# Optimization experiments

Measured on AMD Instinct MI355X. Metric: run time of the kernel, lower is better.

## Reference

```python
import jax, jax.numpy as jnp
import numpy as np

HIDDEN = 1024
HEADS = 16
HEAD_DIM = HIDDEN // HEADS  # 64
MLP_HIDDEN = int(HIDDEN * 4.0)  # 4096
B, L = 2, 2048
EPS_LN = 1e-6
EPS_RMS = 1e-6


def setup_inputs() -> dict:
    key = jax.random.key(0)
    ks = jax.random.split(key, 12)
    s = 0.02
    return {
        "x": jax.random.normal(ks[0], (B, L, HIDDEN), jnp.float32),
        "vec": jax.random.normal(ks[1], (B, HIDDEN), jnp.float32),
        "pe": jax.random.normal(ks[2], (1, 1, L, HEAD_DIM // 2, 2, 2), jnp.float32),
        "w_mod": jax.random.normal(ks[3], (HIDDEN, 3 * HIDDEN), jnp.float32) * s,
        "b_mod": jnp.zeros((3 * HIDDEN,), jnp.float32),
        "w1": jax.random.normal(ks[4], (HIDDEN, 3 * HIDDEN + MLP_HIDDEN), jnp.float32) * s,
        "b1": jnp.zeros((3 * HIDDEN + MLP_HIDDEN,), jnp.float32),
        "w_mlp": jax.random.normal(ks[5], (MLP_HIDDEN, HIDDEN), jnp.float32) * s,
        "b_mlp": jnp.zeros((HIDDEN,), jnp.float32),
        "w2": jax.random.normal(ks[6], (2 * HIDDEN, HIDDEN), jnp.float32) * s,
        "b2": jnp.zeros((HIDDEN,), jnp.float32),
        "q_scale": jnp.ones((HEAD_DIM,), jnp.float32),
        "k_scale": jnp.ones((HEAD_DIM,), jnp.float32),
    }


def _layernorm(x, eps=EPS_LN):
    m = jnp.mean(x, axis=-1, keepdims=True)
    v = jnp.mean(jnp.square(x - m), axis=-1, keepdims=True)
    return (x - m) * jax.lax.rsqrt(v + eps)


def _rmsnorm(x, scale, eps=EPS_RMS):
    rrms = jax.lax.rsqrt(jnp.mean(jnp.square(x), axis=-1, keepdims=True) + eps)
    return x * rrms * scale


def _apply_rope(t, pe):
    # t: [B,H,L,D]; pe: [1,1,L,D//2,2,2]
    t_ = t.reshape(*t.shape[:-1], -1, 1, 2)  # [B,H,L,D//2,1,2]
    out = pe[..., 0] * t_[..., 0] + pe[..., 1] * t_[..., 1]  # [B,H,L,D//2,2]
    return out.reshape(t.shape)


def reference(x, vec, pe, w_mod, b_mod, w1, b1, w_mlp, b_mlp, w2, b2, q_scale, k_scale):
    # adaLN modulation: silu(vec) -> Dense(3*dim) -> shift, scale, gate
    mod = (jax.nn.silu(vec) @ w_mod + b_mod)[:, None, :]  # [B,1,3H]
    shift, scale, gate = jnp.split(mod, 3, axis=-1)
    x_mod = (1.0 + scale) * _layernorm(x) + shift
    # fused QKV + MLP projection
    h = x_mod @ w1 + b1  # [B,L,3H+MH]
    qkv, mlp = h[..., : 3 * HIDDEN], h[..., 3 * HIDDEN :]
    qkv = qkv.reshape(x.shape[0], x.shape[1], 3, HEADS, HEAD_DIM)
    qkv = jnp.transpose(qkv, (2, 0, 3, 1, 4))  # [3,B,H,L,D]
    q, k, v = qkv[0], qkv[1], qkv[2]
    # QK-RMSNorm per head-dim
    q = _rmsnorm(q, q_scale)
    k = _rmsnorm(k, k_scale)
    # RoPE
    q = _apply_rope(q, pe)
    k = _apply_rope(k, pe)
    # attention
    scores = jnp.einsum("bhqd,bhkd->bhqk", q, k) * (HEAD_DIM ** -0.5)
    probs = jax.nn.softmax(scores, axis=-1)
    attn = jnp.einsum("bhqk,bhkd->bhqd", probs, v)
    attn = jnp.transpose(attn, (0, 2, 1, 3)).reshape(x.shape[0], x.shape[1], HIDDEN)
    # mlp branch (Dense with tanh activation per source) + fused output proj
    mlp_out = jnp.tanh(mlp @ w_mlp + b_mlp)
    out = jnp.concatenate([attn, mlp_out], axis=-1) @ w2 + b2
    return x + gate * out
```

## Files before the change

### kernel.cpp

```cpp
#include <hip/hip_runtime.h>
#include <stdint.h>


#define HID  1024
#define NH   16
#define HD   64
#define MLP  4096
#define D1   7168
#define DQKV 3072
#define DCAT 2048
#define BB   2
#define LL   2048
#define TOK  4096

typedef __attribute__((ext_vector_type(8))) short    bf16x8;
typedef __attribute__((ext_vector_type(4))) float    f32x4;
typedef __attribute__((ext_vector_type(4))) unsigned int u32x4;

__device__ __forceinline__ float b2f(unsigned short u) {
    unsigned int v = ((unsigned int)u) << 16;
    float f; __builtin_memcpy(&f, &v, 4); return f;
}
__device__ __forceinline__ unsigned short f2b(float f) {
    unsigned int v; __builtin_memcpy(&v, &f, 4);
    unsigned int r = (v + 0x7FFFu + ((v >> 16) & 1u)) >> 16;
    return (unsigned short)r;
}
__device__ __forceinline__ unsigned int pkbf2(float a, float b) {
    unsigned int ua, ub;
    __builtin_memcpy(&ua, &a, 4); __builtin_memcpy(&ub, &b, 4);
    return ((ua + 0x8000u) >> 16) | ((ub + 0x8000u) & 0xFFFF0000u);
}
__device__ __forceinline__ void gl_lds16(const unsigned short* g, unsigned short* l) {
    __builtin_amdgcn_global_load_lds(
        (const __attribute__((address_space(1))) unsigned int*)(g),
        (__attribute__((address_space(3))) unsigned int*)(l), 16, 0, 0);
}

__global__ void k_transpose_cvt(const float* __restrict__ in,
                                unsigned short* __restrict__ out, int R, int C) {
    __shared__ float tile[32][33];
    int bx = blockIdx.x, by = blockIdx.y;
    int tx = threadIdx.x, ty = threadIdx.y;
    #pragma unroll
    for (int i = 0; i < 4; i++) {
        int r = by * 32 + ty + i * 8;
        int c = bx * 32 + tx;
        tile[ty + i * 8][tx] = in[(size_t)r * C + c];
    }
    __syncthreads();
    #pragma unroll
    for (int i = 0; i < 4; i++) {
        int ro = bx * 32 + ty + i * 8;
        int co = by * 32 + tx;
        out[(size_t)ro * R + co] = f2b(tile[tx][ty + i * 8]);
    }
}

__global__ void k_mod(const float* __restrict__ vec,
                      const float* __restrict__ w_mod,
                      const float* __restrict__ b_mod,
                      float* __restrict__ mod) {
    __shared__ float sv[HID];
    __shared__ float red[8][32];
    int b = blockIdx.y, t = threadIdx.x;
    for (int j = t; j < HID; j += 256) {
        float v = vec[b * HID + j];
        sv[j] = v / (1.0f + __expf(-v));
    }
    __syncthreads();
    int n0 = blockIdx.x * 32;
    int on = t & 31, ks = t >> 5;
    float acc = 0.f;
    const float* wp = w_mod + (size_t)(ks * 128) * 3072 + n0 + on;
    #pragma unroll 4
    for (int k = 0; k < 128; k++) acc += sv[ks * 128 + k] * wp[(size_t)k * 3072];
    red[ks][on] = acc;
    __syncthreads();
    if (t < 32) {
        float s = 0.f;
        #pragma unroll
        for (int i = 0; i < 8; i++) s += red[i][t];
        mod[b * 3072 + n0 + t] = s + b_mod[n0 + t];
    }
}

__global__ void k_lnmod(const float* __restrict__ x,
                        const float* __restrict__ mod,
                        unsigned short* __restrict__ xmod) {
    int tok = blockIdx.x;
    int t = threadIdx.x;
    int b = tok >> 11;
    float4 v4 = *(const float4*)(x + (size_t)tok * HID + t * 4);
    float v0 = v4.x, v1 = v4.y, v2 = v4.z, v3 = v4.w;
    float s  = v0 + v1 + v2 + v3;
    float sq = v0*v0 + v1*v1 + v2*v2 + v3*v3;
    for (int off = 1; off < 64; off <<= 1) {
        s  += __shfl_xor(s,  off);
        sq += __shfl_xor(sq, off);
    }
    __shared__ float ls[4], lq[4];
    int w = t >> 6;
    if ((t & 63) == 0) { ls[w] = s; lq[w] = sq; }
    __syncthreads();
    s  = ls[0] + ls[1] + ls[2] + ls[3];
    sq = lq[0] + lq[1] + lq[2] + lq[3];
    float mean = s * (1.0f / HID);
    float var  = sq * (1.0f / HID) - mean * mean;
    float rstd = rsqrtf(var + 1e-6f);
    const float* mb = mod + b * 3072;
    float y[4] = {v0, v1, v2, v3};
    unsigned short r[4];
    #pragma unroll
    for (int j = 0; j < 4; j++) {
        int col = t * 4 + j;
        float nval = (y[j] - mean) * rstd;
        r[j] = f2b((1.0f + mb[1024 + col]) * nval + mb[col]);
    }
    unsigned int o0 = (unsigned int)r[0] | ((unsigned int)r[1] << 16);
    unsigned int o1 = (unsigned int)r[2] | ((unsigned int)r[3] << 16);
    *(uint2*)(xmod + (size_t)tok * HID + t * 4) = make_uint2(o0, o1);
}

template<int EPI>
__global__ __launch_bounds__(256) void k_gemm(
    const unsigned short* __restrict__ A, int lda,
    const unsigned short* __restrict__ Bt, int ldb,
    const float* __restrict__ bias,
    unsigned short* __restrict__ C, float* __restrict__ Cf, int ldc,
    int K,
    const float* __restrict__ xin,
    const float* __restrict__ mod) {
    __shared__ alignas(16) unsigned short As[128 * 32];
    __shared__ alignas(16) unsigned short Bs[128 * 32];
    int t = threadIdx.x;
    int bm = blockIdx.x, bn = blockIdx.y;
    int lane = t & 63, wave = t >> 6;
    int wm = (wave >> 1) * 64, wn = (wave & 1) * 64;
    int ln = lane & 15, kq = lane >> 4;
    int cs  = (((t & 3) ^ ((t >> 4) & 3)) * 8);
    int kqs = (kq ^ ((ln >> 2) & 3)) * 8;

    f32x4 acc[4][4];
    #pragma unroll
    for (int i = 0; i < 4; i++)
        #pragma unroll
        for (int j = 0; j < 4; j++) acc[i][j] = {0.f, 0.f, 0.f, 0.f};

    int r0 = t >> 2;
    const unsigned short* Ab = A  + (size_t)(bm * 128) * lda;
    const unsigned short* Bb = Bt + (size_t)(bn * 128) * ldb;

    int ksplit = K / gridDim.z;
    int kbeg = blockIdx.z * ksplit, kend = kbeg + ksplit;

    for (int k0 = kbeg; k0 < kend; k0 += 32) {
        __syncthreads();
        gl_lds16(Ab + (size_t)r0 * lda + k0 + cs,        &As[t * 8]);
        gl_lds16(Ab + (size_t)(r0 + 64) * lda + k0 + cs, &As[2048 + t * 8]);
        gl_lds16(Bb + (size_t)r0 * ldb + k0 + cs,        &Bs[t * 8]);
        gl_lds16(Bb + (size_t)(r0 + 64) * ldb + k0 + cs, &Bs[2048 + t * 8]);
        __syncthreads();
        bf16x8 af[4], bfr[4];
        #pragma unroll
        for (int i = 0; i < 4; i++)
            af[i] = *(const bf16x8*)(&As[(wm + i * 16 + ln) * 32 + kqs]);
        #pragma unroll
        for (int j = 0; j < 4; j++)
            bfr[j] = *(const bf16x8*)(&Bs[(wn + j * 16 + ln) * 32 + kqs]);
        #pragma unroll
        for (int i = 0; i < 4; i++)
            #pragma unroll
            for (int j = 0; j < 4; j++)
                acc[i][j] = __builtin_amdgcn_mfma_f32_16x16x32_bf16(af[i], bfr[j], acc[i][j], 0, 0, 0);
    }

    #pragma unroll
    for (int i = 0; i < 4; i++) {
        #pragma unroll
        for (int j = 0; j < 4; j++) {
            int col = bn * 128 + wn + j * 16 + ln;
            float bv = (EPI == 3) ? 0.f : bias[col];
            #pragma unroll
            for (int r = 0; r < 4; r++) {
                int row = bm * 128 + wm + i * 16 + kq * 4 + r;
                float v = acc[i][j][r] + bv;
                if (EPI == 0) {
                    C[(size_t)row * ldc + col] = f2b(v);
                } else if (EPI == 1) {
                    C[(size_t)row * ldc + col] = f2b(tanhf(v));
                } else if (EPI == 2) {
                    int b = row >> 11;
                    Cf[(size_t)row * ldc + col] =
                        xin[(size_t)row * HID + col] + mod[b * 3072 + 2048 + col] * v;
                } else {
                    Cf[((size_t)blockIdx.z * TOK + row) * ldc + col] = v;
                }
            }
        }
    }
}

__global__ __launch_bounds__(256) void k_red1(const float* __restrict__ part,
                                              const float* __restrict__ bias,
                                              unsigned short* __restrict__ cat) {
    int idx = blockIdx.x * 256 + threadIdx.x;
    int row = idx >> 8;
    int c4  = (idx & 255) * 4;
    float4 p0 = *(const float4*)(part + (size_t)row * HID + c4);
    float4 p1 = *(const float4*)(part + ((size_t)TOK + row) * HID + c4);
    float4 bv = *(const float4*)(bias + c4);
    float a0 = tanhf(p0.x + p1.x + bv.x);
    float a1 = tanhf(p0.y + p1.y + bv.y);
    float a2 = tanhf(p0.z + p1.z + bv.z);
    float a3 = tanhf(p0.w + p1.w + bv.w);
    *(uint2*)(&cat[(size_t)row * DCAT + HID + c4]) =
        make_uint2(pkbf2(a0, a1), pkbf2(a2, a3));
}

__global__ __launch_bounds__(256) void k_red2(const float* __restrict__ part,
                                              const float* __restrict__ bias,
                                              const float* __restrict__ x,
                                              const float* __restrict__ mod,
                                              float* __restrict__ out) {
    int idx = blockIdx.x * 256 + threadIdx.x;
    int row = idx >> 8;
    int c4  = (idx & 255) * 4;
    int b = row >> 11;
    float4 p0 = *(const float4*)(part + (size_t)row * HID + c4);
    float4 p1 = *(const float4*)(part + ((size_t)TOK + row) * HID + c4);
    float4 bv = *(const float4*)(bias + c4);
    float4 gv = *(const float4*)(mod + b * 3072 + 2048 + c4);
    float4 xv = *(const float4*)(x + (size_t)row * HID + c4);
    float4 o;
    o.x = xv.x + gv.x * (p0.x + p1.x + bv.x);
    o.y = xv.y + gv.y * (p0.y + p1.y + bv.y);
    o.z = xv.z + gv.z * (p0.z + p1.z + bv.z);
    o.w = xv.w + gv.w * (p0.w + p1.w + bv.w);
    *(float4*)(out + (size_t)row * HID + c4) = o;
}

__global__ void k_qkrope(unsigned short* __restrict__ h,
                         const float* __restrict__ pe,
                         const float* __restrict__ q_scale,
                         const float* __restrict__ k_scale) {
    int tok = blockIdx.x;
    int l = tok & (LL - 1);
    int t = threadIdx.x;
    int lane = t & 63, wave = t >> 6;
    int hh = wave * 4 + (lane >> 4);
    int d0 = (lane & 15) * 4;
    unsigned short* row = h + (size_t)tok * D1;
    int i0 = d0 >> 1;
    const float* peb = pe + ((size_t)l * 32 + i0) * 4;
    float4 e0 = *(const float4*)(peb);
    float4 e1 = *(const float4*)(peb + 4);
    #pragma unroll
    for (int qk = 0; qk < 2; qk++) {
        unsigned short* p = row + qk * HID + hh * HD + d0;
        const float* sc = (qk == 0 ? q_scale : k_scale) + d0;
        uint2 qv = *(const uint2*)p;
        float v0 = b2f((unsigned short)(qv.x & 0xFFFF)), v1 = b2f((unsigned short)(qv.x >> 16));
        float v2 = b2f((unsigned short)(qv.y & 0xFFFF)), v3 = b2f((unsigned short)(qv.y >> 16));
        float ssq = v0*v0 + v1*v1 + v2*v2 + v3*v3;
        ssq += __shfl_xor(ssq, 1, 16);
        ssq += __shfl_xor(ssq, 2, 16);
        ssq += __shfl_xor(ssq, 4, 16);
        ssq += __shfl_xor(ssq, 8, 16);
        float rr = rsqrtf(ssq * (1.0f / HD) + 1e-6f);
        if (qk == 0) rr *= 0.18033688011112042f;
        v0 *= rr * sc[0];
        v1 *= rr * sc[1];
        v2 *= rr * sc[2];
        v3 *= rr * sc[3];
        float o0 = e0.x*v0 + e0.y*v1;
        float o1 = e0.z*v0 + e0.w*v1;
        float o2 = e1.x*v2 + e1.y*v3;
        float o3 = e1.z*v2 + e1.w*v3;
        *(uint2*)p = make_uint2(pkbf2(o0, o1), pkbf2(o2, o3));
    }
}

#define KT 64
#define LDP 72
__global__ __launch_bounds__(256) void k_attn(const unsigned short* __restrict__ h,
                                              unsigned short* __restrict__ cat) {
    __shared__ unsigned short Ks[KT * LDP];
    __shared__ unsigned short Vt[HD * LDP];
    __shared__ unsigned short Ps[4 * 32 * LDP];
    int t = threadIdx.x;
    int bx = blockIdx.x;
    int bh = blockIdx.y;
    int b = bh >> 4, hh = bh & 15;
    int lane = t & 63, w = t >> 6;
    int ln = lane & 15, quad = lane >> 4;
    const unsigned short* hb = h + (size_t)b * LL * D1;

    bf16x8 qf[2][2];
    {
        const unsigned short* qbase = hb + (size_t)(bx * 128 + w * 32) * D1 + hh * HD;
        #pragma unroll
        for (int qt = 0; qt < 2; qt++)
            #pragma unroll
            for (int ks = 0; ks < 2; ks++)
                qf[qt][ks] = *(const bf16x8*)(qbase + (size_t)(qt * 16 + ln) * D1 + ks * 32 + quad * 8);
    }

    f32x4 O[4][2];
    #pragma unroll
    for (int vn = 0; vn < 4; vn++)
        #pragma unroll
        for (int qt = 0; qt < 2; qt++) O[vn][qt] = {0.f, 0.f, 0.f, 0.f};
    float m_[2] = {-1e30f, -1e30f};
    float l_[2] = {0.f, 0.f};

    unsigned short* Psw = Ps + w * 32 * LDP;

    int skey = t >> 2, sdc = (t & 3) * 16;
    int p2 = (t & 31) * 2, db = (t >> 5) * 8;

    for (int kb = 0; kb < LL / KT; kb++) {
        __syncthreads();
        {
            const unsigned short* kbase = hb + (size_t)(kb * KT) * D1 + HID + hh * HD;
            u32x4 ka = *(const u32x4*)(kbase + (size_t)skey * D1 + sdc);
            u32x4 kc = *(const u32x4*)(kbase + (size_t)skey * D1 + sdc + 8);
            *(u32x4*)(&Ks[skey * LDP + sdc]) = ka;
            *(u32x4*)(&Ks[skey * LDP + sdc + 8]) = kc;
            const unsigned short* vbase = hb + (size_t)(kb * KT) * D1 + 2 * HID + hh * HD;
            u32x4 va = *(const u32x4*)(vbase + (size_t)p2 * D1 + db);
            u32x4 vb = *(const u32x4*)(vbase + (size_t)(p2 + 1) * D1 + db);
            #pragma unroll
            for (int j = 0; j < 8; j++) {
                unsigned int lo = (j & 1) ? (va[j >> 1] >> 16) : (va[j >> 1] & 0xFFFFu);
                unsigned int hi = (j & 1) ? (vb[j >> 1] >> 16) : (vb[j >> 1] & 0xFFFFu);
                *(unsigned int*)(&Vt[(db + j) * LDP + p2]) = lo | (hi << 16);
            }
        }
        __syncthreads();

        f32x4 st[4][2];
        #pragma unroll
        for (int kt = 0; kt < 4; kt++) {
            st[kt][0] = {0.f, 0.f, 0.f, 0.f};
            st[kt][1] = {0.f, 0.f, 0.f, 0.f};
            #pragma unroll
            for (int ks = 0; ks < 2; ks++) {
                bf16x8 kf = *(const bf16x8*)(&Ks[(kt * 16 + ln) * LDP + ks * 32 + quad * 8]);
                st[kt][0] = __builtin_amdgcn_mfma_f32_16x16x32_bf16(kf, qf[0][ks], st[kt][0], 0, 0, 0);
                st[kt][1] = __builtin_amdgcn_mfma_f32_16x16x32_bf16(kf, qf[1][ks], st[kt][1], 0, 0, 0);
            }
        }

        #pragma unroll
        for (int qt = 0; qt < 2; qt++) {
            float p[16];
            float mx = -1e30f;
            #pragma unroll
            for (int kt = 0; kt < 4; kt++)
                #pragma unroll
                for (int r = 0; r < 4; r++) {
                    float v = st[kt][qt][r];
                    p[kt * 4 + r] = v;
                    mx = fmaxf(mx, v);
                }
            mx = fmaxf(mx, __shfl_xor(mx, 16));
            mx = fmaxf(mx, __shfl_xor(mx, 32));
            float mnew = fmaxf(m_[qt], mx);
            float alpha = __builtin_amdgcn_exp2f(m_[qt] - mnew);
            m_[qt] = mnew;
            float sum = 0.f;
            #pragma unroll
            for (int i = 0; i < 16; i++) {
                float e = __builtin_amdgcn_exp2f(p[i] - mnew);
                p[i] = e;
                sum += e;
            }
            sum += __shfl_xor(sum, 16);
            sum += __shfl_xor(sum, 32);
            l_[qt] = l_[qt] * alpha + sum;
            #pragma unroll
            for (int vn = 0; vn < 4; vn++)
                #pragma unroll
                for (int r = 0; r < 4; r++) O[vn][qt][r] *= alpha;
            #pragma unroll
            for (int kt = 0; kt < 4; kt++) {
                unsigned long long pk =
                    (unsigned long long)pkbf2(p[kt*4+0], p[kt*4+1])
                  | ((unsigned long long)pkbf2(p[kt*4+2], p[kt*4+3]) << 32);
                *(unsigned long long*)(&Psw[(qt * 16 + ln) * LDP + kt * 16 + quad * 4]) = pk;
            }
        }

        #pragma unroll
        for (int kt2 = 0; kt2 < 2; kt2++) {
            bf16x8 pb0 = *(const bf16x8*)(&Psw[(0  + ln) * LDP + kt2 * 32 + quad * 8]);
            bf16x8 pb1 = *(const bf16x8*)(&Psw[(16 + ln) * LDP + kt2 * 32 + quad * 8]);
            #pragma unroll
            for (int vn = 0; vn < 4; vn++) {
                bf16x8 vf = *(const bf16x8*)(&Vt[(vn * 16 + ln) * LDP + kt2 * 32 + quad * 8]);
                O[vn][0] = __builtin_amdgcn_mfma_f32_16x16x32_bf16(vf, pb0, O[vn][0], 0, 0, 0);
                O[vn][1] = __builtin_amdgcn_mfma_f32_16x16x32_bf16(vf, pb1, O[vn][1], 0, 0, 0);
            }
        }
    }

    #pragma unroll
    for (int qt = 0; qt < 2; qt++) {
        float rl = 1.0f / l_[qt];
        size_t row = (size_t)(b * LL + bx * 128 + w * 32 + qt * 16 + ln);
        #pragma unroll
        for (int vn = 0; vn < 4; vn++) {
            #pragma unroll
            for (int r2 = 0; r2 < 4; r2 += 2) {
                unsigned int pk = pkbf2(O[vn][qt][r2] * rl, O[vn][qt][r2 + 1] * rl);
                *(unsigned int*)(&cat[row * DCAT + hh * HD + vn * 16 + quad * 4 + r2]) = pk;
            }
        }
    }
}

extern "C" void kernel_launch(void* const* d_in, const int* in_sizes, int n_in,
                              void* d_out, int out_size, void* d_ws, size_t ws_size,
                              hipStream_t stream) {
    const float* x       = (const float*)d_in[0];
    const float* vec     = (const float*)d_in[1];
    const float* pe      = (const float*)d_in[2];
    const float* w_mod   = (const float*)d_in[3];
    const float* b_mod   = (const float*)d_in[4];
    const float* w1      = (const float*)d_in[5];
    const float* b1      = (const float*)d_in[6];
    const float* w_mlp   = (const float*)d_in[7];
    const float* b_mlp   = (const float*)d_in[8];
    const float* w2      = (const float*)d_in[9];
    const float* b2      = (const float*)d_in[10];
    const float* q_scale = (const float*)d_in[11];
    const float* k_scale = (const float*)d_in[12];
    float* out = (float*)d_out;

    char* ws = (char*)d_ws;
    size_t off = 0;
    float* mod = (float*)(ws + off);                     off += 6144 * 4;
    unsigned short* xmod  = (unsigned short*)(ws + off); off += (size_t)TOK * HID * 2;
    unsigned short* h     = (unsigned short*)(ws + off); off += (size_t)TOK * D1 * 2;
    unsigned short* cat   = (unsigned short*)(ws + off); off += (size_t)TOK * DCAT * 2;
    unsigned short* w1T   = (unsigned short*)(ws + off); off += (size_t)D1 * HID * 2;
    unsigned short* wmlpT = (unsigned short*)(ws + off); off += (size_t)HID * MLP * 2;
    unsigned short* w2T   = (unsigned short*)(ws + off); off += (size_t)HID * DCAT * 2;
    float* part = (float*)(ws + off);                    off += (size_t)2 * TOK * HID * 4;

    k_transpose_cvt<<<dim3(D1 / 32, HID / 32), dim3(32, 8), 0, stream>>>(w1, w1T, HID, D1);
    k_transpose_cvt<<<dim3(HID / 32, MLP / 32), dim3(32, 8), 0, stream>>>(w_mlp, wmlpT, MLP, HID);
    k_transpose_cvt<<<dim3(HID / 32, DCAT / 32), dim3(32, 8), 0, stream>>>(w2, w2T, DCAT, HID);

    k_mod<<<dim3(96, BB), 256, 0, stream>>>(vec, w_mod, b_mod, mod);
    k_lnmod<<<TOK, 256, 0, stream>>>(x, mod, xmod);

    k_gemm<0><<<dim3(TOK / 128, D1 / 128), 256, 0, stream>>>(
        xmod, HID, w1T, HID, b1, h, nullptr, D1, HID, nullptr, nullptr);

    k_qkrope<<<TOK, 256, 0, stream>>>(h, pe, q_scale, k_scale);

    k_attn<<<dim3(LL / 128, BB * NH), 256, 0, stream>>>(h, cat);

    k_gemm<3><<<dim3(TOK / 128, HID / 128, 2), 256, 0, stream>>>(
        h + DQKV, D1, wmlpT, MLP, b_mlp, nullptr, part, HID, MLP, nullptr, nullptr);
    k_red1<<<TOK * HID / 1024, 256, 0, stream>>>(part, b_mlp, cat);

    k_gemm<3><<<dim3(TOK / 128, HID / 128, 2), 256, 0, stream>>>(
        cat, DCAT, w2T, DCAT, b2, nullptr, part, HID, DCAT, nullptr, nullptr);
    k_red2<<<TOK * HID / 1024, 256, 0, stream>>>(part, b2, x, mod, out);
}
```

Measured before the change: 447.3 us.

## Double GEMM K-tile to 64 with XOR swizzle; shrink attention query tile

The GEMM now stages a 64-wide K slice per iteration with an 8-way XOR swizzle, so there are half as many barrier pairs per unit of MFMA work. The cost is twice the LDS per block, which may lower occupancy. The attention kernel now handles 16 query rows per wave instead of 32 and launches twice as many blocks. That raises parallelism and cuts register use, but each K/V tile loaded into shared memory is reused across half as many queries.

```diff
diff --git a/kernel.cpp b/kernel.cpp
--- a/kernel.cpp
+++ b/kernel.cpp
@@ -131,15 +131,14 @@
     int K,
     const float* __restrict__ xin,
     const float* __restrict__ mod) {
-    __shared__ alignas(16) unsigned short As[128 * 32];
-    __shared__ alignas(16) unsigned short Bs[128 * 32];
+    __shared__ alignas(16) unsigned short As[128 * 64];
+    __shared__ alignas(16) unsigned short Bs[128 * 64];
     int t = threadIdx.x;
     int bm = blockIdx.x, bn = blockIdx.y;
     int lane = t & 63, wave = t >> 6;
     int wm = (wave >> 1) * 64, wn = (wave & 1) * 64;
     int ln = lane & 15, kq = lane >> 4;
-    int cs  = (((t & 3) ^ ((t >> 4) & 3)) * 8);
-    int kqs = (kq ^ ((ln >> 2) & 3)) * 8;
+    int ln7 = ln & 7;
 
     f32x4 acc[4][4];
     #pragma unroll
@@ -147,32 +146,38 @@
         #pragma unroll
         for (int j = 0; j < 4; j++) acc[i][j] = {0.f, 0.f, 0.f, 0.f};
 
-    int r0 = t >> 2;
+    int sr  = t >> 3;
+    int scg = (t & 7) ^ (sr & 7);
     const unsigned short* Ab = A  + (size_t)(bm * 128) * lda;
     const unsigned short* Bb = Bt + (size_t)(bn * 128) * ldb;
 
     int ksplit = K / gridDim.z;
     int kbeg = blockIdx.z * ksplit, kend = kbeg + ksplit;
 
-    for (int k0 = kbeg; k0 < kend; k0 += 32) {
+    for (int k0 = kbeg; k0 < kend; k0 += 64) {
         __syncthreads();
-        gl_lds16(Ab + (size_t)r0 * lda + k0 + cs,        &As[t * 8]);
-        gl_lds16(Ab + (size_t)(r0 + 64) * lda + k0 + cs, &As[2048 + t * 8]);
-        gl_lds16(Bb + (size_t)r0 * ldb + k0 + cs,        &Bs[t * 8]);
-        gl_lds16(Bb + (size_t)(r0 + 64) * ldb + k0 + cs, &Bs[2048 + t * 8]);
+        #pragma unroll
+        for (int c = 0; c < 4; c++) {
+            gl_lds16(Ab + (size_t)(c * 32 + sr) * lda + k0 + scg * 8, &As[c * 2048 + t * 8]);
+            gl_lds16(Bb + (size_t)(c * 32 + sr) * ldb + k0 + scg * 8, &Bs[c * 2048 + t * 8]);
+        }
         __syncthreads();
-        bf16x8 af[4], bfr[4];
-        #pragma unroll
-        for (int i = 0; i < 4; i++)
-            af[i] = *(const bf16x8*)(&As[(wm + i * 16 + ln) * 32 + kqs]);
-        #pragma unroll
-        for (int j = 0; j < 4; j++)
-            bfr[j] = *(const bf16x8*)(&Bs[(wn + j * 16 + ln) * 32 + kqs]);
-        #pragma unroll
-        for (int i = 0; i < 4; i++)
+        #pragma unroll
+        for (int ks = 0; ks < 2; ks++) {
+            int slot = ((ks * 4 + kq) ^ ln7) * 8;
+            bf16x8 af[4], bfr[4];
+            #pragma unroll
+            for (int i = 0; i < 4; i++)
+                af[i] = *(const bf16x8*)(&As[(wm + i * 16 + ln) * 64 + slot]);
             #pragma unroll
             for (int j = 0; j < 4; j++)
-                acc[i][j] = __builtin_amdgcn_mfma_f32_16x16x32_bf16(af[i], bfr[j], acc[i][j], 0, 0, 0);
+                bfr[j] = *(const bf16x8*)(&Bs[(wn + j * 16 + ln) * 64 + slot]);
+            #pragma unroll
+            for (int i = 0; i < 4; i++)
+                #pragma unroll
+                for (int j = 0; j < 4; j++)
+                    acc[i][j] = __builtin_amdgcn_mfma_f32_16x16x32_bf16(af[i], bfr[j], acc[i][j], 0, 0, 0);
+        }
     }
 
     #pragma unroll
@@ -287,7 +292,7 @@
                                               unsigned short* __restrict__ cat) {
     __shared__ unsigned short Ks[KT * LDP];
     __shared__ unsigned short Vt[HD * LDP];
-    __shared__ unsigned short Ps[4 * 32 * LDP];
+    __shared__ unsigned short Ps[4 * 16 * LDP];
     int t = threadIdx.x;
     int bx = blockIdx.x;
     int bh = blockIdx.y;
@@ -296,25 +301,20 @@
     int ln = lane & 15, quad = lane >> 4;
     const unsigned short* hb = h + (size_t)b * LL * D1;
 
-    bf16x8 qf[2][2];
+    bf16x8 qf[2];
     {
-        const unsigned short* qbase = hb + (size_t)(bx * 128 + w * 32) * D1 + hh * HD;
-        #pragma unroll
-        for (int qt = 0; qt < 2; qt++)
-            #pragma unroll
-            for (int ks = 0; ks < 2; ks++)
-                qf[qt][ks] = *(const bf16x8*)(qbase + (size_t)(qt * 16 + ln) * D1 + ks * 32 + quad * 8);
-    }
-
-    f32x4 O[4][2];
-    #pragma unroll
-    for (int vn = 0; vn < 4; vn++)
-        #pragma unroll
-        for (int qt = 0; qt < 2; qt++) O[vn][qt] = {0.f, 0.f, 0.f, 0.f};
-    float m_[2] = {-1e30f, -1e30f};
-    float l_[2] = {0.f, 0.f};
-
-    unsigned short* Psw = Ps + w * 32 * LDP;
+        const unsigned short* qbase = hb + (size_t)(bx * 64 + w * 16) * D1 + hh * HD;
+        #pragma unroll
+        for (int ks = 0; ks < 2; ks++)
+            qf[ks] = *(const bf16x8*)(qbase + (size_t)ln * D1 + ks * 32 + quad * 8);
+    }
+
+    f32x4 O[4];
+    #pragma unroll
+    for (int vn = 0; vn < 4; vn++) O[vn] = {0.f, 0.f, 0.f, 0.f};
+    float m_ = -1e30f, l_ = 0.f;
+
+    unsigned short* Psw = Ps + w * 16 * LDP;
 
     int skey = t >> 2, sdc = (t & 3) * 16;
     int p2 = (t & 31) * 2, db = (t >> 5) * 8;
@@ -339,36 +339,33 @@
         }
         __syncthreads();
 
-        f32x4 st[4][2];
+        f32x4 st[4];
         #pragma unroll
         for (int kt = 0; kt < 4; kt++) {
-            st[kt][0] = {0.f, 0.f, 0.f, 0.f};
-            st[kt][1] = {0.f, 0.f, 0.f, 0.f};
+            st[kt] = {0.f, 0.f, 0.f, 0.f};
             #pragma unroll
             for (int ks = 0; ks < 2; ks++) {
                 bf16x8 kf = *(const bf16x8*)(&Ks[(kt * 16 + ln) * LDP + ks * 32 + quad * 8]);
-                st[kt][0] = __builtin_amdgcn_mfma_f32_16x16x32_bf16(kf, qf[0][ks], st[kt][0], 0, 0, 0);
-                st[kt][1] = __builtin_amdgcn_mfma_f32_16x16x32_bf16(kf, qf[1][ks], st[kt][1], 0, 0, 0);
-            }
-        }
-
-        #pragma unroll
-        for (int qt = 0; qt < 2; qt++) {
+                st[kt] = __builtin_amdgcn_mfma_f32_16x16x32_bf16(kf, qf[ks], st[kt], 0, 0, 0);
+            }
+        }
+
+        {
             float p[16];
             float mx = -1e30f;
             #pragma unroll
             for (int kt = 0; kt < 4; kt++)
                 #pragma unroll
                 for (int r = 0; r < 4; r++) {
-                    float v = st[kt][qt][r];
+                    float v = st[kt][r];
                     p[kt * 4 + r] = v;
                     mx = fmaxf(mx, v);
                 }
             mx = fmaxf(mx, __shfl_xor(mx, 16));
             mx = fmaxf(mx, __shfl_xor(mx, 32));
-            float mnew = fmaxf(m_[qt], mx);
-            float alpha = __builtin_amdgcn_exp2f(m_[qt] - mnew);
-            m_[qt] = mnew;
+            float mnew = fmaxf(m_, mx);
+            float alpha = __builtin_amdgcn_exp2f(m_ - mnew);
+            m_ = mnew;
             float sum = 0.f;
             #pragma unroll
             for (int i = 0; i < 16; i++) {
@@ -378,42 +375,39 @@
             }
             sum += __shfl_xor(sum, 16);
             sum += __shfl_xor(sum, 32);
-            l_[qt] = l_[qt] * alpha + sum;
+            l_ = l_ * alpha + sum;
             #pragma unroll
             for (int vn = 0; vn < 4; vn++)
                 #pragma unroll
-                for (int r = 0; r < 4; r++) O[vn][qt][r] *= alpha;
+                for (int r = 0; r < 4; r++) O[vn][r] *= alpha;
             #pragma unroll
             for (int kt = 0; kt < 4; kt++) {
                 unsigned long long pk =
                     (unsigned long long)pkbf2(p[kt*4+0], p[kt*4+1])
                   | ((unsigned long long)pkbf2(p[kt*4+2], p[kt*4+3]) << 32);
-                *(unsigned long long*)(&Psw[(qt * 16 + ln) * LDP + kt * 16 + quad * 4]) = pk;
+                *(unsigned long long*)(&Psw[ln * LDP + kt * 16 + quad * 4]) = pk;
             }
         }
 
         #pragma unroll
         for (int kt2 = 0; kt2 < 2; kt2++) {
-            bf16x8 pb0 = *(const bf16x8*)(&Psw[(0  + ln) * LDP + kt2 * 32 + quad * 8]);
-            bf16x8 pb1 = *(const bf16x8*)(&Psw[(16 + ln) * LDP + kt2 * 32 + quad * 8]);
+            bf16x8 pb = *(const bf16x8*)(&Psw[ln * LDP + kt2 * 32 + quad * 8]);
             #pragma unroll
             for (int vn = 0; vn < 4; vn++) {
                 bf16x8 vf = *(const bf16x8*)(&Vt[(vn * 16 + ln) * LDP + kt2 * 32 + quad * 8]);
-                O[vn][0] = __builtin_amdgcn_mfma_f32_16x16x32_bf16(vf, pb0, O[vn][0], 0, 0, 0);
-                O[vn][1] = __builtin_amdgcn_mfma_f32_16x16x32_bf16(vf, pb1, O[vn][1], 0, 0, 0);
-            }
-        }
-    }
-
-    #pragma unroll
-    for (int qt = 0; qt < 2; qt++) {
-        float rl = 1.0f / l_[qt];
-        size_t row = (size_t)(b * LL + bx * 128 + w * 32 + qt * 16 + ln);
+                O[vn] = __builtin_amdgcn_mfma_f32_16x16x32_bf16(vf, pb, O[vn], 0, 0, 0);
+            }
+        }
+    }
+
+    {
+        float rl = 1.0f / l_;
+        size_t row = (size_t)(b * LL + bx * 64 + w * 16 + ln);
         #pragma unroll
         for (int vn = 0; vn < 4; vn++) {
             #pragma unroll
             for (int r2 = 0; r2 < 4; r2 += 2) {
-                unsigned int pk = pkbf2(O[vn][qt][r2] * rl, O[vn][qt][r2 + 1] * rl);
+                unsigned int pk = pkbf2(O[vn][r2] * rl, O[vn][r2 + 1] * rl);
                 *(unsigned int*)(&cat[row * DCAT + hh * HD + vn * 16 + quad * 4 + r2]) = pk;
             }
         }
@@ -461,7 +455,7 @@
 
     k_qkrope<<<TOK, 256, 0, stream>>>(h, pe, q_scale, k_scale);
 
-    k_attn<<<dim3(LL / 128, BB * NH), 256, 0, stream>>>(h, cat);
+    k_attn<<<dim3(LL / 64, BB * NH), 256, 0, stream>>>(h, cat);
 
     k_gemm<3><<<dim3(TOK / 128, HID / 128, 2), 256, 0, stream>>>(
         h + DQKV, D1, wmlpT, MLP, b_mlp, nullptr, part, HID, MLP, nullptr, nullptr);
```

Measured after the change: 418.0 us. 6.6% less time.
